# Optimization experiments

Hardware: AMD Instinct MI355X
Metric: run time of the kernel (lower is better)

The kernel has to match this reference:

```python
import jax, jax.numpy as jnp
from jax import lax
import numpy as np

V, E, H = 32000, 32, 8  # vocab, embed dim, hidden dim
S, B = 128, 64          # seq_len, batch


def setup_inputs() -> dict:
    key = jax.random.key(0)
    ks = jax.random.split(key, 16)
    u = lambda k, shape, s: jax.random.uniform(k, shape, jnp.float32, -s, s)
    sH = 1.0 / np.sqrt(H)
    sE = 1.0 / np.sqrt(E)
    sV = 1.0 / np.sqrt(V)
    return {
        "input_batch": jax.random.randint(ks[0], (S, B), 0, V),
        "lookup": u(ks[1], (V, E), sE),
        "weight_xf": u(ks[2], (E, H), sH),
        "weight_hf": u(ks[3], (H, H), sH),
        "weight_xb": u(ks[4], (E, H), sH),
        "weight_hb": u(ks[5], (H, H), sH),
        "weight_o": u(ks[6], (2 * H, V), sV),
        "H_f": u(ks[7], (H,), sH),
        "H_b": u(ks[8], (H,), sH),
        "b_f1": u(ks[9], (H,), sH),
        "b_f2": u(ks[10], (H,), sH),
        "b_b1": u(ks[11], (H,), sH),
        "b_b2": u(ks[12], (H,), sH),
        "b_o": u(ks[13], (V,), sV),
    }


def reference(input_batch, lookup, weight_xf, weight_hf, weight_xb, weight_hb,
              weight_o, H_f, H_b, b_f1, b_f2, b_b1, b_b2, b_o):
    seq, bsz = input_batch.shape
    X = lookup[input_batch]  # [S, B, E]

    # NOTE: the torch code stores the hidden state BEFORE consuming token i
    # (H_f_table[i] = Hf_pre), so scan emits the carry before the update.
    def step_f(h, x):
        h_new = jnp.tanh(x @ weight_xf + b_f1 + h @ weight_hf + b_f2)
        return h_new, h

    def step_b(h, x):
        h_new = jnp.tanh(x @ weight_xb + b_b1 + h @ weight_hb + b_b2)
        return h_new, h

    h0f = jnp.broadcast_to(H_f, (bsz, H))
    h0b = jnp.broadcast_to(H_b, (bsz, H))
    _, Hf_table = lax.scan(step_f, h0f, X)            # [S, B, H] (pre-states)
    _, Hb_rev = lax.scan(step_b, h0b, X[::-1])        # reversed pre-states
    Hb_table = Hb_rev[::-1]                           # [S, B, H]

    Hcat = jnp.concatenate([Hf_table, Hb_table], axis=-1)   # [S, B, 2H]
    logits = jnp.einsum('sbh,hv->sbv', Hcat, weight_o) + b_o
    return jax.nn.log_softmax(logits, axis=-1)
```

## Files before the change

### kernel.cpp

```cpp
#include <hip/hip_runtime.h>

#define SEQ 128
#define BSZ 64
#define EMB 32
#define HD  8
#define VOC 32000
#define NPOS (SEQ * BSZ)
#define NRB  (NPOS / 32)
#define NVS  40
#define TPW  25

typedef float f32x4  __attribute__((ext_vector_type(4)));
typedef short bf16x8 __attribute__((ext_vector_type(8)));
typedef float f32x16 __attribute__((ext_vector_type(16)));

__device__ __forceinline__ unsigned short f2bf(float f) {
    union { float f; unsigned int u; } x; x.f = f;
    unsigned int r = x.u + 0x7fffu + ((x.u >> 16) & 1u);
    return (unsigned short)(r >> 16);
}

__global__ __launch_bounds__(256) void prep_kernel(
    const int*   __restrict__ idx,
    const float* __restrict__ lookup,
    const float* __restrict__ Wxf, const float* __restrict__ Wxb,
    const float* __restrict__ bf1, const float* __restrict__ bf2,
    const float* __restrict__ bb1, const float* __restrict__ bb2,
    const float* __restrict__ Wo,
    float* __restrict__ xpf, float* __restrict__ xpb,
    unsigned short* __restrict__ wt)
{
    if (blockIdx.x < 32) {
        const int i = blockIdx.x * 256 + threadIdx.x;
        const int s = i >> 6;
        const int b = i & 63;

        const float* xr = lookup + (size_t)idx[i] * EMB;
        float x[EMB];
#pragma unroll
        for (int e = 0; e < EMB; ++e) x[e] = xr[e];

#pragma unroll
        for (int h = 0; h < HD; ++h) {
            float af = bf1[h] + bf2[h];
            float ab = bb1[h] + bb2[h];
#pragma unroll
            for (int e = 0; e < EMB; ++e) {
                af = fmaf(x[e], Wxf[e * HD + h], af);
                ab = fmaf(x[e], Wxb[e * HD + h], ab);
            }
            xpf[(b * HD + h) * SEQ + s]             = af;
            xpb[(b * HD + h) * SEQ + (SEQ - 1 - s)] = ab;
        }
    } else {
        const int v = (blockIdx.x - 32) * 256 + threadIdx.x;
        if (v < VOC) {
#pragma unroll
            for (int k = 0; k < 16; ++k)
                wt[v * 16 + k] = f2bf(Wo[k * VOC + v]);
        }
    }
}

__global__ __launch_bounds__(512) void rnn_scan_kernel(
    const float* __restrict__ xpf, const float* __restrict__ xpb,
    const float* __restrict__ Whf, const float* __restrict__ Whb,
    const float* __restrict__ Hf0, const float* __restrict__ Hb0,
    unsigned short* __restrict__ hc2)
{
    const int dir = blockIdx.x;
    const int tid = threadIdx.x;
    const int b   = tid >> 3;
    const int h   = tid & 7;

    const float* Wh = dir ? Whb : Whf;
    const float* xp = (dir ? xpb : xpf) + (size_t)tid * SEQ;

    float wh[HD];
#pragma unroll
    for (int j = 0; j < HD; ++j) wh[j] = Wh[j * HD + h];

    float xs[SEQ];
    const f32x4* xp4 = (const f32x4*)xp;
#pragma unroll
    for (int q = 0; q < SEQ / 4; ++q) {
        f32x4 v = xp4[q];
        xs[4 * q + 0] = v.x; xs[4 * q + 1] = v.y;
        xs[4 * q + 2] = v.z; xs[4 * q + 3] = v.w;
    }

    float hcur = dir ? Hb0[h] : Hf0[h];
    const int koff = dir ? HD : 0;

#pragma unroll
    for (int t = 0; t < SEQ; ++t) {
        const int s = dir ? (SEQ - 1 - t) : t;
        hc2[(s * BSZ + b) * 16 + koff + h] = f2bf(hcur);

        float acc = xs[t];
#pragma unroll
        for (int j = 0; j < HD; ++j)
            acc = fmaf(__shfl(hcur, j, 8), wh[j], acc);

        float e = __expf(2.0f * acc);
        hcur = (e - 1.0f) / (e + 1.0f);
    }
}

__global__ __launch_bounds__(256) void lse_partial_kernel(
    const unsigned short* __restrict__ hc2,
    const unsigned short* __restrict__ wt,
    const float* __restrict__ bo,
    float* __restrict__ partial)
{
    const int gw   = blockIdx.x * 4 + (threadIdx.x >> 6);
    const int rb   = gw / NVS;
    const int vs   = gw - rb * NVS;
    const int lane = threadIdx.x & 63;
    const int half = lane >> 5;
    const int lc   = lane & 31;

    const bf16x8 afrag = *(const bf16x8*)(hc2 + (size_t)(rb * 32 + lc) * 16 + half * 8);

    f32x16 zv;
#pragma unroll
    for (int i = 0; i < 16; ++i) zv[i] = 0.0f;

    float sacc[16];
#pragma unroll
    for (int g = 0; g < 16; ++g) sacc[g] = 0.0f;

    for (int t = 0; t < TPW; ++t) {
        const int v0 = (vs * TPW + t) * 32;
        const bf16x8 bfrag = *(const bf16x8*)(wt + (size_t)(v0 + lc) * 16 + half * 8);
        f32x16 d = __builtin_amdgcn_mfma_f32_32x32x16_bf16(afrag, bfrag, zv, 0, 0, 0);
        const float bov = bo[v0 + lc];
#pragma unroll
        for (int g = 0; g < 16; ++g)
            sacc[g] += __expf(d[g] + bov);
    }

#pragma unroll
    for (int g = 0; g < 16; ++g) {
        float s = sacc[g];
        s += __shfl_xor(s, 1, 32);
        s += __shfl_xor(s, 2, 32);
        s += __shfl_xor(s, 4, 32);
        s += __shfl_xor(s, 8, 32);
        s += __shfl_xor(s, 16, 32);
        sacc[g] = s;
    }

    if (lc == 0) {
#pragma unroll
        for (int g = 0; g < 16; ++g) {
            const int row = (g & 3) + 8 * (g >> 2) + 4 * half;
            partial[(size_t)(rb * 32 + row) * NVS + vs] = sacc[g];
        }
    }
}

__global__ __launch_bounds__(256) void lse_reduce_kernel(
    const float* __restrict__ partial, float* __restrict__ lse)
{
    const int row = blockIdx.x * 256 + threadIdx.x;
    if (row >= NPOS) return;
    const f32x4* p4 = (const f32x4*)(partial + (size_t)row * NVS);
    float s = 0.0f;
#pragma unroll
    for (int q = 0; q < NVS / 4; ++q) {
        f32x4 v = p4[q];
        s += v.x + v.y + v.z + v.w;
    }
    lse[row] = logf(s);
}

__global__ __launch_bounds__(256) void out_mfma_kernel(
    const unsigned short* __restrict__ hc2,
    const unsigned short* __restrict__ wt,
    const float* __restrict__ bo,
    const float* __restrict__ lse,
    float* __restrict__ out)
{
    const int gw   = blockIdx.x * 4 + (threadIdx.x >> 6);
    const int rb   = gw / NVS;
    const int vs   = gw - rb * NVS;
    const int lane = threadIdx.x & 63;
    const int half = lane >> 5;
    const int lc   = lane & 31;

    const bf16x8 afrag = *(const bf16x8*)(hc2 + (size_t)(rb * 32 + lc) * 16 + half * 8);

    f32x16 zv;
#pragma unroll
    for (int i = 0; i < 16; ++i) zv[i] = 0.0f;

    float lse16[16];
#pragma unroll
    for (int g = 0; g < 16; ++g) {
        const int row = (g & 3) + 8 * (g >> 2) + 4 * half;
        lse16[g] = lse[rb * 32 + row];
    }

    for (int t = 0; t < TPW; ++t) {
        const int v0 = (vs * TPW + t) * 32;
        const bf16x8 bfrag = *(const bf16x8*)(wt + (size_t)(v0 + lc) * 16 + half * 8);
        f32x16 d = __builtin_amdgcn_mfma_f32_32x32x16_bf16(afrag, bfrag, zv, 0, 0, 0);
        const float bov = bo[v0 + lc];
#pragma unroll
        for (int g = 0; g < 16; ++g) {
            const int row = (g & 3) + 8 * (g >> 2) + 4 * half;
            const float val = d[g] + bov - lse16[g];
            __builtin_nontemporal_store(
                val, out + (size_t)(rb * 32 + row) * VOC + v0 + lc);
        }
    }
}

extern "C" void kernel_launch(void* const* d_in, const int* in_sizes, int n_in,
                              void* d_out, int out_size, void* d_ws, size_t ws_size,
                              hipStream_t stream)
{
    const int*   idx    = (const int*)  d_in[0];
    const float* lookup = (const float*)d_in[1];
    const float* Wxf    = (const float*)d_in[2];
    const float* Whf    = (const float*)d_in[3];
    const float* Wxb    = (const float*)d_in[4];
    const float* Whb    = (const float*)d_in[5];
    const float* Wo     = (const float*)d_in[6];
    const float* Hf0    = (const float*)d_in[7];
    const float* Hb0    = (const float*)d_in[8];
    const float* bf1    = (const float*)d_in[9];
    const float* bf2    = (const float*)d_in[10];
    const float* bb1    = (const float*)d_in[11];
    const float* bb2    = (const float*)d_in[12];
    const float* bo     = (const float*)d_in[13];
    float* out = (float*)d_out;

    char* ws = (char*)d_ws;
    float*          xpf     = (float*)ws;          ws += BSZ * HD * SEQ * 4;
    float*          xpb     = (float*)ws;          ws += BSZ * HD * SEQ * 4;
    unsigned short* hc2     = (unsigned short*)ws; ws += NPOS * 16 * 2;
    unsigned short* wt      = (unsigned short*)ws; ws += VOC * 16 * 2;
    float*          partial = (float*)ws;          ws += (size_t)NPOS * NVS * 4;
    float*          lse     = (float*)ws;          ws += NPOS * 4;

    hipLaunchKernelGGL(prep_kernel, dim3(32 + VOC / 256), dim3(256), 0, stream,
                       idx, lookup, Wxf, Wxb, bf1, bf2, bb1, bb2, Wo,
                       xpf, xpb, wt);
    hipLaunchKernelGGL(rnn_scan_kernel, dim3(2), dim3(512), 0, stream,
                       xpf, xpb, Whf, Whb, Hf0, Hb0, hc2);
    hipLaunchKernelGGL(lse_partial_kernel, dim3(NRB * NVS / 4), dim3(256), 0, stream,
                       hc2, wt, bo, partial);
    hipLaunchKernelGGL(lse_reduce_kernel, dim3(NPOS / 256), dim3(256), 0, stream,
                       partial, lse);
    hipLaunchKernelGGL(out_mfma_kernel, dim3(NRB * NVS / 4), dim3(256), 0, stream,
                       hc2, wt, bo, lse, out);
}
```

Measured before the change: 290.8 us.

## Retile output kernel to hold vocab fragments in registers across row blocks

The output kernel now gives each wave 4 vocab tiles, whose weight fragments and biases stay in registers, and loops over 16 row blocks, instead of one row block over 25 vocab tiles. Each write instruction still covers 32 consecutive columns in 16 rows, but a wave now writes 128 columns wide across 512 rows. The nontemporal stores are replaced with ordinary stores. This trades weight reuse for more hc2 and lse loads, and changes the write pattern to the 1 GB output, which may help or hurt DRAM write efficiency.

```diff
diff --git a/kernel.cpp b/kernel.cpp
--- a/kernel.cpp
+++ b/kernel.cpp
@@ -7,8 +7,13 @@
 #define VOC 32000
 #define NPOS (SEQ * BSZ)
 #define NRB  (NPOS / 32)
+#define NTILE (VOC / 32)
 #define NVS  40
 #define TPW  25
+#define VTW  4
+#define NVG  (NTILE / VTW)
+#define RBW  16
+#define NRG  (NRB / RBW)
 
 typedef float f32x4  __attribute__((ext_vector_type(4)));
 typedef short bf16x8 __attribute__((ext_vector_type(8)));
@@ -182,37 +187,51 @@
     const float* __restrict__ lse,
     float* __restrict__ out)
 {
-    const int gw   = blockIdx.x * 4 + (threadIdx.x >> 6);
-    const int rb   = gw / NVS;
-    const int vs   = gw - rb * NVS;
+    const int w    = threadIdx.x >> 6;
+    const int gw   = blockIdx.x * 4 + w;
+    const int vg   = gw % NVG;
+    const int rg   = gw / NVG;
     const int lane = threadIdx.x & 63;
     const int half = lane >> 5;
     const int lc   = lane & 31;
 
-    const bf16x8 afrag = *(const bf16x8*)(hc2 + (size_t)(rb * 32 + lc) * 16 + half * 8);
+    bf16x8 bfr[VTW];
+    float  bov[VTW];
+#pragma unroll
+    for (int t = 0; t < VTW; ++t) {
+        const int v0 = (vg * VTW + t) * 32;
+        bfr[t] = *(const bf16x8*)(wt + (size_t)(v0 + lc) * 16 + half * 8);
+        bov[t] = bo[v0 + lc];
+    }
 
     f32x16 zv;
 #pragma unroll
     for (int i = 0; i < 16; ++i) zv[i] = 0.0f;
 
-    float lse16[16];
-#pragma unroll
-    for (int g = 0; g < 16; ++g) {
-        const int row = (g & 3) + 8 * (g >> 2) + 4 * half;
-        lse16[g] = lse[rb * 32 + row];
-    }
-
-    for (int t = 0; t < TPW; ++t) {
-        const int v0 = (vs * TPW + t) * 32;
-        const bf16x8 bfrag = *(const bf16x8*)(wt + (size_t)(v0 + lc) * 16 + half * 8);
-        f32x16 d = __builtin_amdgcn_mfma_f32_32x32x16_bf16(afrag, bfrag, zv, 0, 0, 0);
-        const float bov = bo[v0 + lc];
+    const int vbase = vg * VTW * 32;
+
+    for (int r = 0; r < RBW; ++r) {
+        const int rb = rg * RBW + r;
+
+        const bf16x8 afrag =
+            *(const bf16x8*)(hc2 + (size_t)(rb * 32 + lc) * 16 + half * 8);
+
+        float nls[16];
 #pragma unroll
         for (int g = 0; g < 16; ++g) {
             const int row = (g & 3) + 8 * (g >> 2) + 4 * half;
-            const float val = d[g] + bov - lse16[g];
-            __builtin_nontemporal_store(
-                val, out + (size_t)(rb * 32 + row) * VOC + v0 + lc);
+            nls[g] = -lse[rb * 32 + row];
+        }
+
+#pragma unroll
+        for (int t = 0; t < VTW; ++t) {
+            f32x16 d = __builtin_amdgcn_mfma_f32_32x32x16_bf16(afrag, bfr[t], zv, 0, 0, 0);
+#pragma unroll
+            for (int g = 0; g < 16; ++g) {
+                const int row = (g & 3) + 8 * (g >> 2) + 4 * half;
+                const float val = d[g] + bov[t] + nls[g];
+                *(out + (size_t)(rb * 32 + row) * VOC + vbase + t * 32 + lc) = val;
+            }
         }
     }
 }
@@ -254,6 +273,6 @@
                        hc2, wt, bo, partial);
     hipLaunchKernelGGL(lse_reduce_kernel, dim3(NPOS / 256), dim3(256), 0, stream,
                        partial, lse);
-    hipLaunchKernelGGL(out_mfma_kernel, dim3(NRB * NVS / 4), dim3(256), 0, stream,
+    hipLaunchKernelGGL(out_mfma_kernel, dim3(NVG * NRG / 4), dim3(256), 0, stream,
                        hc2, wt, bo, lse, out);
 }
```

Measured after the change: 284.8 us. -2.1%, faster.
